# Kernel optimization log

Hardware: AMD Instinct MI355X
Metric: run time of the kernel (lower is better)

The kernel has to match this reference:

```python
import jax, jax.numpy as jnp
import numpy as np

B, S, D = 2, 2048, 4096
NH, NKV, HD = 32, 8, 128
GROUPS = NH // NKV
SCALE = HD ** -0.5


def _rotate_half(x):
    x1, x2 = x[..., : HD // 2], x[..., HD // 2 :]
    return jnp.concatenate((-x2, x1), axis=-1)


def setup_inputs() -> dict:
    key = jax.random.key(0)
    ks = jax.random.split(key, 6)
    hidden_states = jax.random.normal(ks[0], (B, S, D), dtype=jnp.float32)
    # Real RoPE tables: cos/sin of shape [B, S, HD]
    inv_freq = 1.0 / (10000.0 ** (jnp.arange(0, HD, 2, dtype=jnp.float32) / HD))
    pos = jnp.arange(S, dtype=jnp.float32)
    freqs = pos[:, None] * inv_freq[None, :]            # [S, HD/2]
    emb = jnp.concatenate((freqs, freqs), axis=-1)       # [S, HD]
    cos = jnp.broadcast_to(jnp.cos(emb)[None], (B, S, HD))
    sin = jnp.broadcast_to(jnp.sin(emb)[None], (B, S, HD))
    std = D ** -0.5
    wq = jax.random.normal(ks[1], (NH * HD, D), dtype=jnp.float32) * std
    wk = jax.random.normal(ks[2], (NKV * HD, D), dtype=jnp.float32) * std
    wv = jax.random.normal(ks[3], (NKV * HD, D), dtype=jnp.float32) * std
    wo = jax.random.normal(ks[4], (D, NH * HD), dtype=jnp.float32) * std
    return {"hidden_states": hidden_states, "cos": cos, "sin": sin,
            "wq": wq, "wk": wk, "wv": wv, "wo": wo}


def reference(hidden_states, cos, sin, wq, wk, wv, wo):
    bsz, q_len, _ = hidden_states.shape
    # projections (nn.Linear: y = x @ W.T), reshape to [B, H, S, HD]
    q = (hidden_states @ wq.T).reshape(bsz, q_len, NH, HD).transpose(0, 2, 1, 3)
    k = (hidden_states @ wk.T).reshape(bsz, q_len, NKV, HD).transpose(0, 2, 1, 3)
    v = (hidden_states @ wv.T).reshape(bsz, q_len, NKV, HD).transpose(0, 2, 1, 3)
    # RoPE, cos/sin broadcast over head dim
    c, s = cos[:, None], sin[:, None]
    q = q * c + _rotate_half(q) * s
    k = k * c + _rotate_half(k) * s
    # GQA repeat_kv: [B, NKV, S, HD] -> [B, NH, S, HD]
    k = jnp.repeat(k, GROUPS, axis=1)
    v = jnp.repeat(v, GROUPS, axis=1)
    scores = jnp.einsum("bhqd,bhkd->bhqk", q, k) * SCALE
    causal = jnp.triu(jnp.ones((q_len, q_len), dtype=bool), k=1)
    scores = jnp.where(causal[None, None], -jnp.inf, scores)
    attn = jax.nn.softmax(scores.astype(jnp.float32), axis=-1).astype(q.dtype)
    out = jnp.einsum("bhqk,bhkd->bhqd", attn, v)
    out = out.transpose(0, 2, 1, 3).reshape(bsz, q_len, NH * HD)
    return out @ wo.T
```

## Files before the change

kernel.cpp:

```cpp
#include <hip/hip_runtime.h>

#define B_    2
#define S_    2048
#define D_    4096
#define NH_   32
#define NKV_  8
#define HD_   128
#define M_TOK 4096
#define NQKV  6144
#define SCALE 0.08838834764831845f

typedef unsigned short u16;
typedef unsigned int   u32;
typedef __attribute__((ext_vector_type(8))) short short8;
typedef __attribute__((ext_vector_type(4))) float floatx4;
typedef __attribute__((ext_vector_type(16))) float floatx16;

typedef const __attribute__((address_space(1))) void cg_void;
typedef __attribute__((address_space(3))) void lds_void;
#define GP(x) ((cg_void*)(x))
#define LP(x) ((lds_void*)(x))

__device__ inline u16 f2bf(float f) {
    u32 u = __float_as_uint(f);
    u = (u + 0x7FFFu + ((u >> 16) & 1u)) >> 16;
    return (u16)u;
}
__device__ inline float bf2f(u16 u) {
    return __uint_as_float(((u32)u) << 16);
}

__global__ __launch_bounds__(256) void cvt_bf16(
    const float* __restrict__ src, u16* __restrict__ dst, int n8)
{
    int id = blockIdx.x * 256 + threadIdx.x;
    if (id >= n8) return;
    size_t i = (size_t)id * 8;
    float4 a = *(const float4*)(src + i);
    float4 b = *(const float4*)(src + i + 4);
    __align__(16) u16 t[8];
    t[0] = f2bf(a.x); t[1] = f2bf(a.y); t[2] = f2bf(a.z); t[3] = f2bf(a.w);
    t[4] = f2bf(b.x); t[5] = f2bf(b.y); t[6] = f2bf(b.z); t[7] = f2bf(b.w);
    *(short8*)(dst + i) = *(short8*)t;
}

#define GBK 64
#define A_U16 (256 * GBK)
#define B_U16 (128 * GBK)
#define BUF_U16 (A_U16 + B_U16)

template<bool OUT_F32>
__global__ __launch_bounds__(512) void gemm_pipe(
    const u16* __restrict__ A, const u16* __restrict__ Bw,
    void* __restrict__ Cp, int M, int N, int K)
{
    __shared__ __align__(16) u16 smem[2][BUF_U16];

    const int tid  = threadIdx.x;
    const int lane = tid & 63, wave = tid >> 6;
    const int quad = lane >> 4, l16 = lane & 15;

    const int gx  = gridDim.x;
    const int lin = blockIdx.y * gx + blockIdx.x;
    const int nwg = gx * gridDim.y;
    const int wg  = (lin & 7) * (nwg >> 3) + (lin >> 3);
    const int by  = wg / gx, bx = wg - by * gx;
    const int m0 = by * 256, n0 = bx * 128;

    const int wm = (wave >> 1) * 64;
    const int wn = (wave & 1) * 64;

    const int srow  = tid >> 3;
    const int sslot = tid & 7;
    const u16* Asrc = A  + (size_t)(m0 + srow) * K + (size_t)((sslot ^ (srow & 7)) * 8);
    const u16* Bsrc = Bw + (size_t)(n0 + srow) * K + (size_t)((sslot ^ (srow & 7)) * 8);

    const int NT = K / GBK;
    const int sw = l16 & 7;

    floatx4 acc[4][4];
    #pragma unroll
    for (int i = 0; i < 4; ++i)
        #pragma unroll
        for (int j = 0; j < 4; ++j) acc[i][j] = (floatx4){0.f, 0.f, 0.f, 0.f};

    #pragma unroll
    for (int tb = 0; tb < 2; ++tb) {
        u16* Ad = &smem[tb][0]     + tid * 8;
        u16* Bd = &smem[tb][A_U16] + tid * 8;
        const size_t k0 = (size_t)tb * GBK;
        #pragma unroll
        for (int q = 0; q < 4; ++q)
            __builtin_amdgcn_global_load_lds(GP(Asrc + (size_t)q * 64 * K + k0),
                                             LP(Ad + q * 4096), 16, 0, 0);
        #pragma unroll
        for (int q = 0; q < 2; ++q)
            __builtin_amdgcn_global_load_lds(GP(Bsrc + (size_t)q * 64 * K + k0),
                                             LP(Bd + q * 4096), 16, 0, 0);
    }
    __builtin_amdgcn_sched_barrier(0);
    asm volatile("s_waitcnt vmcnt(6)" ::: "memory");
    __builtin_amdgcn_sched_barrier(0);
    __builtin_amdgcn_s_barrier();

    #pragma unroll 1
    for (int t = 0; t < NT; ++t) {
        const u16* Ab = &smem[t & 1][0]     + (size_t)(wm + l16) * GBK;
        const u16* Bb = &smem[t & 1][A_U16] + (size_t)(wn + l16) * GBK;

        #pragma unroll
        for (int kh = 0; kh < 2; ++kh) {
            const int sl = ((kh * 4 + quad) ^ sw) * 8;
            short8 af[4], bfv[4];
            #pragma unroll
            for (int i = 0; i < 4; ++i)
                af[i] = *(const short8*)(Ab + i * 16 * GBK + sl);
            #pragma unroll
            for (int j = 0; j < 4; ++j)
                bfv[j] = *(const short8*)(Bb + j * 16 * GBK + sl);

            __builtin_amdgcn_s_barrier();
            __builtin_amdgcn_s_setprio(1);
            #pragma unroll
            for (int i = 0; i < 4; ++i)
                #pragma unroll
                for (int j = 0; j < 4; ++j)
                    acc[i][j] = __builtin_amdgcn_mfma_f32_16x16x32_bf16(
                        af[i], bfv[j], acc[i][j], 0, 0, 0);
            __builtin_amdgcn_s_setprio(0);
            __builtin_amdgcn_s_barrier();
        }

        if (t + 1 == NT) break;

        __builtin_amdgcn_sched_barrier(0);
        if (t + 2 < NT) {
            u16* Ad = &smem[t & 1][0]     + tid * 8;
            u16* Bd = &smem[t & 1][A_U16] + tid * 8;
            const size_t k0 = (size_t)(t + 2) * GBK;
            #pragma unroll
            for (int q = 0; q < 4; ++q)
                __builtin_amdgcn_global_load_lds(GP(Asrc + (size_t)q * 64 * K + k0),
                                                 LP(Ad + q * 4096), 16, 0, 0);
            #pragma unroll
            for (int q = 0; q < 2; ++q)
                __builtin_amdgcn_global_load_lds(GP(Bsrc + (size_t)q * 64 * K + k0),
                                                 LP(Bd + q * 4096), 16, 0, 0);
            __builtin_amdgcn_sched_barrier(0);
            asm volatile("s_waitcnt vmcnt(6)" ::: "memory");
        } else {
            asm volatile("s_waitcnt vmcnt(0)" ::: "memory");
        }
        __builtin_amdgcn_sched_barrier(0);
        __builtin_amdgcn_s_barrier();
    }

    #pragma unroll
    for (int i = 0; i < 4; ++i)
        #pragma unroll
        for (int j = 0; j < 4; ++j)
            #pragma unroll
            for (int r = 0; r < 4; ++r) {
                int row = m0 + wm + i * 16 + quad * 4 + r;
                int col = n0 + wn + j * 16 + l16;
                float v = acc[i][j][r];
                if constexpr (OUT_F32)
                    ((float*)Cp)[(size_t)row * N + col] = v;
                else
                    ((u16*)Cp)[(size_t)row * N + col] = f2bf(v);
            }
}

__global__ __launch_bounds__(256) void rope_reshape(
    const u16* __restrict__ qkv, const float* __restrict__ cosp,
    const float* __restrict__ sinp, u16* __restrict__ Q, u16* __restrict__ Kb)
{
    const size_t QN = (size_t)M_TOK * NH_ * 64;
    size_t id = (size_t)blockIdx.x * 256 + threadIdx.x;
    if (id < QN) {
        int j = id & 63; int h = (id >> 6) & (NH_ - 1); int tok = (int)(id >> 11);
        int b = tok >> 11, s = tok & (S_ - 1);
        float c  = cosp[(size_t)tok * HD_ + j];
        float sn = sinp[(size_t)tok * HD_ + j];
        float x1 = bf2f(qkv[(size_t)tok * NQKV + h * HD_ + j]);
        float x2 = bf2f(qkv[(size_t)tok * NQKV + h * HD_ + 64 + j]);
        size_t o = ((size_t)(b * NH_ + h) * S_ + s) * HD_ + j;
        Q[o]      = f2bf(x1 * c - x2 * sn);
        Q[o + 64] = f2bf(x2 * c + x1 * sn);
    } else {
        size_t kid = id - QN;
        int j = kid & 63; int h = (kid >> 6) & (NKV_ - 1); int tok = (int)(kid >> 9);
        int b = tok >> 11, s = tok & (S_ - 1);
        float c  = cosp[(size_t)tok * HD_ + j];
        float sn = sinp[(size_t)tok * HD_ + j];
        float x1 = bf2f(qkv[(size_t)tok * NQKV + 4096 + h * HD_ + j]);
        float x2 = bf2f(qkv[(size_t)tok * NQKV + 4096 + h * HD_ + 64 + j]);
        size_t o = ((size_t)(b * NKV_ + h) * S_ + s) * HD_ + j;
        Kb[o]      = f2bf(x1 * c - x2 * sn);
        Kb[o + 64] = f2bf(x2 * c + x1 * sn);
    }
}

__global__ __launch_bounds__(256) void v_transpose(
    const u16* __restrict__ qkv, u16* __restrict__ Vt)
{
    __shared__ __align__(16) u16 T[128][136];
    int bidx = blockIdx.x;
    int st = bidx & 15; int h = (bidx >> 4) & 7; int b = bidx >> 7;
    int s0 = st * 128;
    int tid = threadIdx.x;
    #pragma unroll
    for (int i = 0; i < 8; ++i) {
        int row = i * 16 + (tid >> 4); int cg = tid & 15;
        const u16* src = qkv + (size_t)(b * S_ + s0 + row) * NQKV + 5120 + h * HD_ + cg * 8;
        *(short8*)&T[row][cg * 8] = *(const short8*)src;
    }
    __syncthreads();
    #pragma unroll
    for (int i = 0; i < 8; ++i) {
        int d = i * 16 + (tid >> 4); int cg = tid & 15;
        __align__(16) u16 tmp[8];
        #pragma unroll
        for (int j = 0; j < 8; ++j) tmp[j] = T[cg * 8 + j][d];
        *(short8*)(Vt + ((size_t)(b * NKV_ + h) * HD_ + d) * S_ + s0 + cg * 8) =
            *(short8*)tmp;
    }
}

__global__ __launch_bounds__(256) void flash_attn(
    const u16* __restrict__ Q, const u16* __restrict__ Kb,
    const u16* __restrict__ Vt, u16* __restrict__ AO)
{
    const int tid  = threadIdx.x;
    const int wave = tid >> 6, lane = tid & 63;
    const int l31 = lane & 31, hi = lane >> 5;

    const int i    = blockIdx.x;
    const int xcd  = i & 7;
    const int slot = i >> 3;
    const int g    = slot & 3;
    const int qb   = 15 - ((slot >> 2) & 15);
    const int b    = slot >> 6;
    const int hk   = xcd;
    const int h    = hk * 4 + g;
    const int qt   = qb * 4 + wave;
    const int q0   = qt * 32;
    const int qpos = q0 + l31;

    const u16* Kbase = Kb + (size_t)(b * NKV_ + hk) * S_ * HD_;
    const u16* Vbase = Vt + (size_t)(b * NKV_ + hk) * HD_ * S_;

    const u16* Qp = Q + ((size_t)(b * NH_ + h) * S_ + q0 + l31) * HD_ + hi * 8;
    short8 qf[8];
    #pragma unroll
    for (int c = 0; c < 8; ++c) qf[c] = *(const short8*)(Qp + c * 16);

    float m = -1e30f, l = 0.f;
    floatx16 o[4];
    #pragma unroll
    for (int n = 0; n < 4; ++n)
        #pragma unroll
        for (int r = 0; r < 16; ++r) o[n][r] = 0.f;

    const u16* Kp = Kbase + (size_t)l31 * HD_ + hi * 8;
    const u16* Vp = Vbase + (size_t)l31 * S_ + hi * 8;

    for (int t = 0; t <= qt; ++t) {
        const int kb = t * 32;
        const u16* Kt = Kp + (size_t)kb * HD_;

        floatx16 ca, cb;
        #pragma unroll
        for (int r = 0; r < 16; ++r) { ca[r] = 0.f; cb[r] = 0.f; }
        __builtin_amdgcn_s_setprio(1);
        #pragma unroll
        for (int c = 0; c < 8; c += 2) {
            ca = __builtin_amdgcn_mfma_f32_32x32x16_bf16(
                *(const short8*)(Kt + c * 16), qf[c], ca, 0, 0, 0);
            cb = __builtin_amdgcn_mfma_f32_32x32x16_bf16(
                *(const short8*)(Kt + (c + 1) * 16), qf[c + 1], cb, 0, 0, 0);
        }
        __builtin_amdgcn_s_setprio(0);

        float s[16];
        #pragma unroll
        for (int r = 0; r < 16; ++r) s[r] = ca[r] + cb[r];

        if (t == qt) {
            #pragma unroll
            for (int r = 0; r < 16; ++r) {
                const int kvr = (r & 3) + 8 * (r >> 2) + 4 * hi;
                if (kb + kvr > qpos) s[r] = -1e38f;
            }
        }

        float b0 = fmaxf(fmaxf(s[0], s[1]), fmaxf(s[2], s[3]));
        float b1 = fmaxf(fmaxf(s[4], s[5]), fmaxf(s[6], s[7]));
        float b2 = fmaxf(fmaxf(s[8], s[9]), fmaxf(s[10], s[11]));
        float b3 = fmaxf(fmaxf(s[12], s[13]), fmaxf(s[14], s[15]));
        float bm = fmaxf(fmaxf(b0, b1), fmaxf(b2, b3));
        bm = fmaxf(bm, __shfl_xor(bm, 32));
        const float bmS = bm * SCALE;

        if (__any(bmS > m)) {
            const float mn = fmaxf(m, bmS);
            const float al = __expf(m - mn);
            m = mn;
            l *= al;
            #pragma unroll
            for (int n = 0; n < 4; ++n)
                #pragma unroll
                for (int r = 0; r < 16; ++r) o[n][r] *= al;
        }

        float p[16];
        float rs = 0.f;
        #pragma unroll
        for (int r = 0; r < 16; ++r) {
            p[r] = __expf(fmaf(s[r], SCALE, -m));
            rs += p[r];
        }
        rs += __shfl_xor(rs, 32);
        l += rs;

        u32 P01 = (u32)f2bf(p[0])  | ((u32)f2bf(p[1])  << 16);
        u32 P23 = (u32)f2bf(p[2])  | ((u32)f2bf(p[3])  << 16);
        u32 P45 = (u32)f2bf(p[4])  | ((u32)f2bf(p[5])  << 16);
        u32 P67 = (u32)f2bf(p[6])  | ((u32)f2bf(p[7])  << 16);
        u32 P89 = (u32)f2bf(p[8])  | ((u32)f2bf(p[9])  << 16);
        u32 Pab = (u32)f2bf(p[10]) | ((u32)f2bf(p[11]) << 16);
        u32 Pcd = (u32)f2bf(p[12]) | ((u32)f2bf(p[13]) << 16);
        u32 Pef = (u32)f2bf(p[14]) | ((u32)f2bf(p[15]) << 16);
        u32 x1 = __shfl_xor(hi ? P01 : P45, 32);
        u32 x2 = __shfl_xor(hi ? P23 : P67, 32);
        u32 x3 = __shfl_xor(hi ? P89 : Pcd, 32);
        u32 x4 = __shfl_xor(hi ? Pab : Pef, 32);

        union { short8 v; u32 w[4]; } f0, f1;
        f0.w[0] = hi ? x1 : P01;  f0.w[1] = hi ? x2 : P23;
        f0.w[2] = hi ? P45 : x1;  f0.w[3] = hi ? P67 : x2;
        f1.w[0] = hi ? x3 : P89;  f1.w[1] = hi ? x4 : Pab;
        f1.w[2] = hi ? Pcd : x3;  f1.w[3] = hi ? Pef : x4;

        const u16* Vtp = Vp + kb;
        __builtin_amdgcn_s_setprio(1);
        #pragma unroll
        for (int n = 0; n < 4; ++n) {
            o[n] = __builtin_amdgcn_mfma_f32_32x32x16_bf16(
                *(const short8*)(Vtp + (size_t)(n * 32) * S_), f0.v, o[n], 0, 0, 0);
            o[n] = __builtin_amdgcn_mfma_f32_32x32x16_bf16(
                *(const short8*)(Vtp + (size_t)(n * 32) * S_ + 16), f1.v, o[n], 0, 0, 0);
        }
        __builtin_amdgcn_s_setprio(0);
    }

    const float inv = 1.0f / l;
    u16* dst = AO + ((size_t)(b * S_) + q0 + l31) * (NH_ * HD_) + h * HD_ + hi * 4;
    #pragma unroll
    for (int n = 0; n < 4; ++n)
        #pragma unroll
        for (int rg = 0; rg < 4; ++rg) {
            u32 lo  = (u32)f2bf(o[n][rg * 4 + 0] * inv) |
                      ((u32)f2bf(o[n][rg * 4 + 1] * inv) << 16);
            u32 hi2 = (u32)f2bf(o[n][rg * 4 + 2] * inv) |
                      ((u32)f2bf(o[n][rg * 4 + 3] * inv) << 16);
            *(uint2*)(dst + n * 32 + rg * 8) = make_uint2(lo, hi2);
        }
}

extern "C" void kernel_launch(void* const* d_in, const int* in_sizes, int n_in,
                              void* d_out, int out_size, void* d_ws, size_t ws_size,
                              hipStream_t stream)
{
    const float* hs   = (const float*)d_in[0];
    const float* cosp = (const float*)d_in[1];
    const float* sinp = (const float*)d_in[2];
    const float* wq   = (const float*)d_in[3];
    const float* wk   = (const float*)d_in[4];
    const float* wv   = (const float*)d_in[5];
    const float* wo   = (const float*)d_in[6];
    float* out = (float*)d_out;
    char* ws = (char*)d_ws;

    const size_t MB = 1024 * 1024;
    u16* qkv_raw = (u16*)ws;
    u16* AO      = (u16*)ws;
    u16* Wqkv    = (u16*)(ws + 48 * MB);
    u16* Qb      = (u16*)(ws + 48 * MB);
    u16* Kb      = (u16*)(ws + 80 * MB);
    u16* Vt      = (u16*)(ws + 88 * MB);
    u16* hs_bf   = (u16*)(ws + 96 * MB);
    u16* Wo_bf   = (u16*)(ws + 96 * MB);

    cvt_bf16<<<8192, 256, 0, stream>>>(hs, hs_bf, (M_TOK * D_) / 8);
    cvt_bf16<<<8192, 256, 0, stream>>>(wq, Wqkv, (NH_ * HD_ * D_) / 8);
    cvt_bf16<<<2048, 256, 0, stream>>>(wk, Wqkv + (size_t)NH_ * HD_ * D_, (NKV_ * HD_ * D_) / 8);
    cvt_bf16<<<2048, 256, 0, stream>>>(wv, Wqkv + (size_t)(NH_ + NKV_) * HD_ * D_, (NKV_ * HD_ * D_) / 8);

    gemm_pipe<false><<<dim3(NQKV / 128, M_TOK / 256), 512, 0, stream>>>(
        hs_bf, Wqkv, qkv_raw, M_TOK, NQKV, D_);

    rope_reshape<<<40960, 256, 0, stream>>>(qkv_raw, cosp, sinp, Qb, Kb);

    v_transpose<<<256, 256, 0, stream>>>(qkv_raw, Vt);

    flash_attn<<<1024, 256, 0, stream>>>(Qb, Kb, Vt, AO);

    cvt_bf16<<<8192, 256, 0, stream>>>(wo, Wo_bf, (D_ * NH_ * HD_) / 8);

    gemm_pipe<true><<<dim3(D_ / 128, M_TOK / 256), 512, 0, stream>>>(
        AO, Wo_bf, out, M_TOK, D_, NH_ * HD_);
}
```

Baseline: 882.1 us.

## Stage K/V tiles in LDS with double-buffered async loads in flash attention

The flash attention kernel now loads each 32-key K tile and V^T tile once per workgroup into a double-buffered LDS region using global_load_lds. Before, each of the four waves read K/V straight from global memory per MFMA. Block barriers sync the waves, and the next tile is prefetched while the current one is computed. Waves with fewer causal tiles now idle through the extra iterations. Separately, bf16 packing switches to the hardware v_cvt_pk_bf16_f32 instruction in place of manual rounding.

New measurement: 785.9 us. 1.12x faster.

```diff
diff --git a/kernel.cpp b/kernel.cpp
--- a/kernel.cpp
+++ b/kernel.cpp
@@ -28,6 +28,11 @@
 }
 __device__ inline float bf2f(u16 u) {
     return __uint_as_float(((u32)u) << 16);
+}
+__device__ inline u32 cvt_pk_bf16(float a, float b) {
+    u32 r;
+    asm("v_cvt_pk_bf16_f32 %0, %1, %2" : "=v"(r) : "v"(a), "v"(b));
+    return r;
 }
 
 __global__ __launch_bounds__(256) void cvt_bf16(
@@ -231,6 +236,8 @@
     const u16* __restrict__ Q, const u16* __restrict__ Kb,
     const u16* __restrict__ Vt, u16* __restrict__ AO)
 {
+    __shared__ __align__(16) u16 smem[2][8192];
+
     const int tid  = threadIdx.x;
     const int wave = tid >> 6, lane = tid & 63;
     const int l31 = lane & 31, hi = lane >> 5;
@@ -246,6 +253,7 @@
     const int qt   = qb * 4 + wave;
     const int q0   = qt * 32;
     const int qpos = q0 + l31;
+    const int TB   = qb * 4 + 4;
 
     const u16* Kbase = Kb + (size_t)(b * NKV_ + hk) * S_ * HD_;
     const u16* Vbase = Vt + (size_t)(b * NKV_ + hk) * HD_ * S_;
@@ -254,6 +262,33 @@
     short8 qf[8];
     #pragma unroll
     for (int c = 0; c < 8; ++c) qf[c] = *(const short8*)(Qp + c * 16);
+    __builtin_amdgcn_sched_barrier(0);
+    asm volatile("s_waitcnt vmcnt(0)" ::: "memory");
+    __builtin_amdgcn_sched_barrier(0);
+
+    const int gk0 = tid, gk1 = tid + 256;
+    const int kdsl0 = gk0 >> 5, kkv0 = gk0 & 31;
+    const int kdsl1 = gk1 >> 5, kkv1 = gk1 & 31;
+    const int vks0 = gk0 >> 7, vd0 = gk0 & 127;
+    const int vks1 = gk1 >> 7, vd1 = gk1 & 127;
+
+    #define STAGE_KV(kb_, buf_)                                                        \
+        do {                                                                           \
+            u16* Ksd = &smem[buf_][0];                                                 \
+            u16* Vsd = &smem[buf_][4096];                                              \
+            __builtin_amdgcn_global_load_lds(                                          \
+                GP(Kbase + (size_t)((kb_) + kkv0) * HD_ + kdsl0 * 8),                  \
+                LP(Ksd + gk0 * 8), 16, 0, 0);                                          \
+            __builtin_amdgcn_global_load_lds(                                          \
+                GP(Kbase + (size_t)((kb_) + kkv1) * HD_ + kdsl1 * 8),                  \
+                LP(Ksd + gk1 * 8), 16, 0, 0);                                          \
+            __builtin_amdgcn_global_load_lds(                                          \
+                GP(Vbase + (size_t)vd0 * S_ + (kb_) + vks0 * 8),                       \
+                LP(Vsd + gk0 * 8), 16, 0, 0);                                          \
+            __builtin_amdgcn_global_load_lds(                                          \
+                GP(Vbase + (size_t)vd1 * S_ + (kb_) + vks1 * 8),                       \
+                LP(Vsd + gk1 * 8), 16, 0, 0);                                          \
+        } while (0)
 
     float m = -1e30f, l = 0.f;
     floatx16 o[4];
@@ -262,97 +297,122 @@
         #pragma unroll
         for (int r = 0; r < 16; ++r) o[n][r] = 0.f;
 
-    const u16* Kp = Kbase + (size_t)l31 * HD_ + hi * 8;
-    const u16* Vp = Vbase + (size_t)l31 * S_ + hi * 8;
-
-    for (int t = 0; t <= qt; ++t) {
-        const int kb = t * 32;
-        const u16* Kt = Kp + (size_t)kb * HD_;
-
-        floatx16 ca, cb;
-        #pragma unroll
-        for (int r = 0; r < 16; ++r) { ca[r] = 0.f; cb[r] = 0.f; }
-        __builtin_amdgcn_s_setprio(1);
-        #pragma unroll
-        for (int c = 0; c < 8; c += 2) {
-            ca = __builtin_amdgcn_mfma_f32_32x32x16_bf16(
-                *(const short8*)(Kt + c * 16), qf[c], ca, 0, 0, 0);
-            cb = __builtin_amdgcn_mfma_f32_32x32x16_bf16(
-                *(const short8*)(Kt + (c + 1) * 16), qf[c + 1], cb, 0, 0, 0);
+    STAGE_KV(0, 0);
+    STAGE_KV(32, 1);
+    __builtin_amdgcn_sched_barrier(0);
+    asm volatile("s_waitcnt vmcnt(4)" ::: "memory");
+    __builtin_amdgcn_sched_barrier(0);
+    __builtin_amdgcn_s_barrier();
+
+    #pragma unroll 1
+    for (int t = 0; t < TB; ++t) {
+        const u16* Ks = &smem[t & 1][0];
+        const u16* Vs = &smem[t & 1][4096];
+
+        if (t <= qt) {
+            const int kb = t * 32;
+
+            floatx16 ca, cb;
+            #pragma unroll
+            for (int r = 0; r < 16; ++r) { ca[r] = 0.f; cb[r] = 0.f; }
+            __builtin_amdgcn_s_setprio(1);
+            #pragma unroll
+            for (int c = 0; c < 8; c += 2) {
+                ca = __builtin_amdgcn_mfma_f32_32x32x16_bf16(
+                    *(const short8*)(Ks + (2 * c + hi) * 256 + l31 * 8),
+                    qf[c], ca, 0, 0, 0);
+                cb = __builtin_amdgcn_mfma_f32_32x32x16_bf16(
+                    *(const short8*)(Ks + (2 * (c + 1) + hi) * 256 + l31 * 8),
+                    qf[c + 1], cb, 0, 0, 0);
+            }
+            __builtin_amdgcn_s_setprio(0);
+
+            float s[16];
+            #pragma unroll
+            for (int r = 0; r < 16; ++r) s[r] = ca[r] + cb[r];
+
+            if (t == qt) {
+                #pragma unroll
+                for (int r = 0; r < 16; ++r) {
+                    const int kvr = (r & 3) + 8 * (r >> 2) + 4 * hi;
+                    if (kb + kvr > qpos) s[r] = -1e38f;
+                }
+            }
+
+            float b0 = fmaxf(fmaxf(s[0], s[1]), fmaxf(s[2], s[3]));
+            float b1 = fmaxf(fmaxf(s[4], s[5]), fmaxf(s[6], s[7]));
+            float b2 = fmaxf(fmaxf(s[8], s[9]), fmaxf(s[10], s[11]));
+            float b3 = fmaxf(fmaxf(s[12], s[13]), fmaxf(s[14], s[15]));
+            float bm = fmaxf(fmaxf(b0, b1), fmaxf(b2, b3));
+            bm = fmaxf(bm, __shfl_xor(bm, 32));
+            const float bmS = bm * SCALE;
+
+            if (__any(bmS > m)) {
+                const float mn = fmaxf(m, bmS);
+                const float al = __expf(m - mn);
+                m = mn;
+                l *= al;
+                #pragma unroll
+                for (int n = 0; n < 4; ++n)
+                    #pragma unroll
+                    for (int r = 0; r < 16; ++r) o[n][r] *= al;
+            }
+
+            float p[16];
+            float rs = 0.f;
+            #pragma unroll
+            for (int r = 0; r < 16; ++r) {
+                p[r] = __expf(fmaf(s[r], SCALE, -m));
+                rs += p[r];
+            }
+            rs += __shfl_xor(rs, 32);
+            l += rs;
+
+            u32 P01 = cvt_pk_bf16(p[0],  p[1]);
+            u32 P23 = cvt_pk_bf16(p[2],  p[3]);
+            u32 P45 = cvt_pk_bf16(p[4],  p[5]);
+            u32 P67 = cvt_pk_bf16(p[6],  p[7]);
+            u32 P89 = cvt_pk_bf16(p[8],  p[9]);
+            u32 Pab = cvt_pk_bf16(p[10], p[11]);
+            u32 Pcd = cvt_pk_bf16(p[12], p[13]);
+            u32 Pef = cvt_pk_bf16(p[14], p[15]);
+            u32 x1 = __shfl_xor(hi ? P01 : P45, 32);
+            u32 x2 = __shfl_xor(hi ? P23 : P67, 32);
+            u32 x3 = __shfl_xor(hi ? P89 : Pcd, 32);
+            u32 x4 = __shfl_xor(hi ? Pab : Pef, 32);
+
+            union { short8 v; u32 w[4]; } f0, f1;
+            f0.w[0] = hi ? x1 : P01;  f0.w[1] = hi ? x2 : P23;
+            f0.w[2] = hi ? P45 : x1;  f0.w[3] = hi ? P67 : x2;
+            f1.w[0] = hi ? x3 : P89;  f1.w[1] = hi ? x4 : Pab;
+            f1.w[2] = hi ? Pcd : x3;  f1.w[3] = hi ? Pef : x4;
+
+            __builtin_amdgcn_s_setprio(1);
+            #pragma unroll
+            for (int n = 0; n < 4; ++n) {
+                o[n] = __builtin_amdgcn_mfma_f32_32x32x16_bf16(
+                    *(const short8*)(Vs + (hi) * 1024 + (n * 32 + l31) * 8),
+                    f0.v, o[n], 0, 0, 0);
+                o[n] = __builtin_amdgcn_mfma_f32_32x32x16_bf16(
+                    *(const short8*)(Vs + (2 + hi) * 1024 + (n * 32 + l31) * 8),
+                    f1.v, o[n], 0, 0, 0);
+            }
+            __builtin_amdgcn_s_setprio(0);
         }
-        __builtin_amdgcn_s_setprio(0);
-
-        float s[16];
-        #pragma unroll
-        for (int r = 0; r < 16; ++r) s[r] = ca[r] + cb[r];
-
-        if (t == qt) {
-            #pragma unroll
-            for (int r = 0; r < 16; ++r) {
-                const int kvr = (r & 3) + 8 * (r >> 2) + 4 * hi;
-                if (kb + kvr > qpos) s[r] = -1e38f;
-            }
+
+        __builtin_amdgcn_s_barrier();
+        __builtin_amdgcn_sched_barrier(0);
+        if (t + 2 < TB) {
+            STAGE_KV((t + 2) * 32, t & 1);
+            __builtin_amdgcn_sched_barrier(0);
+            asm volatile("s_waitcnt vmcnt(4)" ::: "memory");
+        } else if (t + 1 < TB) {
+            asm volatile("s_waitcnt vmcnt(0)" ::: "memory");
         }
-
-        float b0 = fmaxf(fmaxf(s[0], s[1]), fmaxf(s[2], s[3]));
-        float b1 = fmaxf(fmaxf(s[4], s[5]), fmaxf(s[6], s[7]));
-        float b2 = fmaxf(fmaxf(s[8], s[9]), fmaxf(s[10], s[11]));
-        float b3 = fmaxf(fmaxf(s[12], s[13]), fmaxf(s[14], s[15]));
-        float bm = fmaxf(fmaxf(b0, b1), fmaxf(b2, b3));
-        bm = fmaxf(bm, __shfl_xor(bm, 32));
-        const float bmS = bm * SCALE;
-
-        if (__any(bmS > m)) {
-            const float mn = fmaxf(m, bmS);
-            const float al = __expf(m - mn);
-            m = mn;
-            l *= al;
-            #pragma unroll
-            for (int n = 0; n < 4; ++n)
-                #pragma unroll
-                for (int r = 0; r < 16; ++r) o[n][r] *= al;
-        }
-
-        float p[16];
-        float rs = 0.f;
-        #pragma unroll
-        for (int r = 0; r < 16; ++r) {
-            p[r] = __expf(fmaf(s[r], SCALE, -m));
-            rs += p[r];
-        }
-        rs += __shfl_xor(rs, 32);
-        l += rs;
-
-        u32 P01 = (u32)f2bf(p[0])  | ((u32)f2bf(p[1])  << 16);
-        u32 P23 = (u32)f2bf(p[2])  | ((u32)f2bf(p[3])  << 16);
-        u32 P45 = (u32)f2bf(p[4])  | ((u32)f2bf(p[5])  << 16);
-        u32 P67 = (u32)f2bf(p[6])  | ((u32)f2bf(p[7])  << 16);
-        u32 P89 = (u32)f2bf(p[8])  | ((u32)f2bf(p[9])  << 16);
-        u32 Pab = (u32)f2bf(p[10]) | ((u32)f2bf(p[11]) << 16);
-        u32 Pcd = (u32)f2bf(p[12]) | ((u32)f2bf(p[13]) << 16);
-        u32 Pef = (u32)f2bf(p[14]) | ((u32)f2bf(p[15]) << 16);
-        u32 x1 = __shfl_xor(hi ? P01 : P45, 32);
-        u32 x2 = __shfl_xor(hi ? P23 : P67, 32);
-        u32 x3 = __shfl_xor(hi ? P89 : Pcd, 32);
-        u32 x4 = __shfl_xor(hi ? Pab : Pef, 32);
-
-        union { short8 v; u32 w[4]; } f0, f1;
-        f0.w[0] = hi ? x1 : P01;  f0.w[1] = hi ? x2 : P23;
-        f0.w[2] = hi ? P45 : x1;  f0.w[3] = hi ? P67 : x2;
-        f1.w[0] = hi ? x3 : P89;  f1.w[1] = hi ? x4 : Pab;
-        f1.w[2] = hi ? Pcd : x3;  f1.w[3] = hi ? Pef : x4;
-
-        const u16* Vtp = Vp + kb;
-        __builtin_amdgcn_s_setprio(1);
-        #pragma unroll
-        for (int n = 0; n < 4; ++n) {
-            o[n] = __builtin_amdgcn_mfma_f32_32x32x16_bf16(
-                *(const short8*)(Vtp + (size_t)(n * 32) * S_), f0.v, o[n], 0, 0, 0);
-            o[n] = __builtin_amdgcn_mfma_f32_32x32x16_bf16(
-                *(const short8*)(Vtp + (size_t)(n * 32) * S_ + 16), f1.v, o[n], 0, 0, 0);
-        }
-        __builtin_amdgcn_s_setprio(0);
-    }
+        __builtin_amdgcn_sched_barrier(0);
+        __builtin_amdgcn_s_barrier();
+    }
+    #undef STAGE_KV
 
     const float inv = 1.0f / l;
     u16* dst = AO + ((size_t)(b * S_) + q0 + l31) * (NH_ * HD_) + h * HD_ + hi * 4;
@@ -360,10 +420,8 @@
     for (int n = 0; n < 4; ++n)
         #pragma unroll
         for (int rg = 0; rg < 4; ++rg) {
-            u32 lo  = (u32)f2bf(o[n][rg * 4 + 0] * inv) |
-                      ((u32)f2bf(o[n][rg * 4 + 1] * inv) << 16);
-            u32 hi2 = (u32)f2bf(o[n][rg * 4 + 2] * inv) |
-                      ((u32)f2bf(o[n][rg * 4 + 3] * inv) << 16);
+            u32 lo  = cvt_pk_bf16(o[n][rg * 4 + 0] * inv, o[n][rg * 4 + 1] * inv);
+            u32 hi2 = cvt_pk_bf16(o[n][rg * 4 + 2] * inv, o[n][rg * 4 + 3] * inv);
             *(uint2*)(dst + n * 32 + rg * 8) = make_uint2(lo, hi2);
         }
 }
```
